# Kernel tuning notes

Measured on AMD Instinct MI355X. Metric: run time of the kernel, lower is better.

## Reference

```python
import jax, jax.numpy as jnp
import numpy as np

EDGES_1B = [[1,2],[1,39],[2,3],[2,25],[3,4],[3,18],[4,5],[4,14],[5,6],[5,8],[6,7],[6,11],[7,8],[8,9],[9,39],[10,11],[10,13],[11,12],[13,14],[14,15],[15,16],[16,17],[16,19],[16,24],[17,18],[17,27],[19,20],[19,33],[20,21],[20,34],[21,22],[22,23],[22,35],[23,24],[23,36],[25,26],[25,37],[26,27],[26,28],[26,29],[28,29],[29,38],[30,38],[31,32],[33,34],[35,36]]
NUM_GRAPHS = 8192
NODES_PER_GRAPH = 39
HIDDEN = 128
NODE_F, EDGE_F, OUT_F = 4, 2, 2
EPS = 1e-5


def _build_edge_index():
    e0 = np.array([[u - 1, v - 1] for u, v in EDGES_1B], dtype=np.int64)
    e = np.concatenate([e0, e0[:, ::-1]], axis=0).T  # [2, 92] bidirectional
    off = np.arange(NUM_GRAPHS, dtype=np.int64) * NODES_PER_GRAPH
    ei = (e[:, None, :] + off[None, :, None]).reshape(2, -1)  # [2, 8192*92]
    return jnp.asarray(ei)


def setup_inputs() -> dict:
    key = jax.random.key(0)
    ks = jax.random.split(key, 16)
    N = NUM_GRAPHS * NODES_PER_GRAPH
    E = NUM_GRAPHS * 92

    def lin(k, fi, fo):
        k1, k2 = jax.random.split(k)
        s = 1.0 / np.sqrt(fi)
        return (jax.random.uniform(k1, (fi, fo), jnp.float32, -s, s),
                jax.random.uniform(k2, (fo,), jnp.float32, -s, s))

    W1a, b1a = lin(ks[0], 2 * NODE_F + EDGE_F, HIDDEN)
    W1b, b1b = lin(ks[1], HIDDEN, HIDDEN)
    W2a, b2a = lin(ks[2], 2 * HIDDEN + EDGE_F, HIDDEN)
    W2b, b2b = lin(ks[3], HIDDEN, HIDDEN)
    Wo, bo = lin(ks[4], HIDDEN, OUT_F)
    return {
        'x': jax.random.normal(ks[5], (N, NODE_F), jnp.float32),
        'edge_index': _build_edge_index(),
        'edge_attr': jax.random.normal(ks[6], (E, EDGE_F), jnp.float32),
        'W1a': W1a, 'b1a': b1a, 'W1b': W1b, 'b1b': b1b,
        'g1': jnp.ones((HIDDEN,), jnp.float32), 'be1': jnp.zeros((HIDDEN,), jnp.float32),
        'W2a': W2a, 'b2a': b2a, 'W2b': W2b, 'b2b': b2b,
        'g2': jnp.ones((HIDDEN,), jnp.float32), 'be2': jnp.zeros((HIDDEN,), jnp.float32),
        'Wo': Wo, 'bo': bo,
    }


def _gnn_layer(x, src, dst, edge_attr, Wa, ba, Wb, bb):
    # message: mlp(cat[x_i, x_j, edge_attr]) with x_i = target, x_j = source
    m = jnp.concatenate([x[dst], x[src], edge_attr], axis=1)  # [E, 2F+Fe]
    m = jax.nn.relu(m @ Wa + ba) @ Wb + bb                    # [E, H]
    N = x.shape[0]
    agg = jax.ops.segment_sum(m, dst, num_segments=N)         # scatter-sum
    cnt = jax.ops.segment_sum(jnp.ones((m.shape[0],), m.dtype), dst, num_segments=N)
    return agg / jnp.maximum(cnt, 1.0)[:, None]               # mean aggregation


def _batch_norm(x, gamma, beta):
    mu = jnp.mean(x, axis=0)
    var = jnp.mean(jnp.square(x - mu), axis=0)  # biased var (training-mode BN)
    return (x - mu) * jax.lax.rsqrt(var + EPS) * gamma + beta


def reference(x, edge_index, edge_attr, W1a, b1a, W1b, b1b, g1, be1,
              W2a, b2a, W2b, b2b, g2, be2, Wo, bo):
    src, dst = edge_index[0], edge_index[1]
    h = _gnn_layer(x, src, dst, edge_attr, W1a, b1a, W1b, b1b)
    h = jax.nn.relu(_batch_norm(h, g1, be1))
    h = _gnn_layer(h, src, dst, edge_attr, W2a, b2a, W2b, b2b)
    h = jax.nn.relu(_batch_norm(h, g2, be2))
    return h @ Wo + bo
```

## Files before the change

### kernel.cpp

```cpp
#include <hip/hip_runtime.h>
#include <hip/hip_bf16.h>

#define NG 8192
#define NPG 39
#define H 128
#define NTOT (NG*NPG)
#define INV_N (1.0f/319488.0f)
#define SHS 136
#define ES 40

typedef __attribute__((ext_vector_type(8))) short bf16x8;
typedef __attribute__((ext_vector_type(8))) unsigned short u16x8;
typedef __attribute__((ext_vector_type(4))) float f32x4;
typedef unsigned short u16;

__device__ __forceinline__ float u16tof(u16 u) {
  union { unsigned int i; float f; } v; v.i = ((unsigned int)u) << 16; return v.f;
}
__device__ __forceinline__ u16 ftou16(float f) {
  union { float f; unsigned int i; } v; v.f = f;
  const unsigned int x = v.i;
  return (u16)((x + 0x7FFFu + ((x >> 16) & 1u)) >> 16);
}
__device__ __forceinline__ unsigned int pk2(float lo, float hi) {
  return (unsigned int)ftou16(lo) | ((unsigned int)ftou16(hi) << 16);
}

__constant__ int INC_OFF[40] = {0,2,5,8,11,14,17,19,22,24,26,29,30,32,35,37,41,44,46,49,
                                52,54,57,60,62,65,69,71,73,76,77,78,79,81,83,85,87,88,90,92};
__constant__ int INC_EID[92] = {
 46,47, 0,48,49, 2,50,51, 4,52,53, 6,54,55, 8,56,57, 10,58, 9,12,59, 13,60,
 61,62, 11,15,63, 17, 16,64, 7,18,65, 19,66, 20,67,68,69, 21,70,71, 5,24,
 22,72,73, 26,74,75, 28,76, 30,77,78, 31,79,80, 23,33, 3,81,82, 35,83,84,85,
 25,37, 38,86, 39,40,87, 88, 89, 43, 27,90, 29,44, 32,91, 34,45, 36, 41,42, 1,14};
__constant__ int INC_SRC[92] = {
 1,38, 0,2,24, 1,3,17, 2,4,13, 3,5,7, 4,6,10, 5,7, 4,6,8, 7,38,
 10,12, 5,9,11, 10, 9,13, 3,12,14, 13,15, 14,16,18,23, 15,17,26, 2,16,
 15,19,32, 18,20,33, 19,21, 20,22,34, 21,23,35, 15,22, 1,25,36, 24,26,27,28,
 16,25, 25,28, 25,27,37, 37, 31, 30, 18,33, 19,32, 21,35, 22,34, 24, 28,29, 0,8};
__constant__ int EDST[92] = {
 1,38,2,24,3,17,4,13,5,7,6,10,7,8,38,10,12,11,13,14,15,16,18,23,17,26,19,32,20,33,21,22,34,23,35,25,36,26,27,28,28,37,37,31,33,35,
 0,0,1,1,2,2,3,3,4,4,5,5,6,7,8,9,9,10,12,13,14,15,15,15,16,16,18,18,19,19,20,21,21,22,22,24,24,25,25,25,27,28,29,30,32,34};
__constant__ int ESRC[92] = {
 0,0,1,1,2,2,3,3,4,4,5,5,6,7,8,9,9,10,12,13,14,15,15,15,16,16,18,18,19,19,20,21,21,22,22,24,24,25,25,25,27,28,29,30,32,34,
 1,38,2,24,3,17,4,13,5,7,6,10,7,8,38,10,12,11,13,14,15,16,18,23,17,26,19,32,20,33,21,22,34,23,35,25,36,26,27,28,28,37,37,31,33,35};
__constant__ float DEGINV[39] = {
 0.5f, 1.f/3, 1.f/3, 1.f/3, 1.f/3, 1.f/3, 0.5f, 1.f/3, 0.5f, 0.5f,
 1.f/3, 1.f,   0.5f, 1.f/3, 0.5f, 0.25f, 1.f/3, 0.5f, 1.f/3, 1.f/3,
 0.5f, 1.f/3, 1.f/3, 0.5f, 1.f/3, 0.25f, 0.5f, 0.5f, 1.f/3, 1.f,
 1.f,  1.f,   0.5f, 0.5f, 0.5f, 0.5f, 1.f,  0.5f, 0.5f};

__global__ __launch_bounds__(256)
void k_tr(const float* __restrict__ W2a, const float* __restrict__ W2b,
          const float* __restrict__ W1b, const float* __restrict__ W1a,
          u16* __restrict__ WT)
{
  const int idx = blockIdx.x * 256 + threadIdx.x;
  if (idx < 65536) {
    const int mat = idx >> 14, rem = idx & 16383;
    const int n = rem >> 7, k = rem & 127;
    float v;
    if (mat == 0)      v = W2a[k*H + n];
    else if (mat == 1) v = W2a[(128 + k)*H + n];
    else if (mat == 2) v = W2b[k*H + n];
    else               v = W1b[k*H + n];
    WT[mat*16384 + n*128 + k] = ftou16(v);
  } else if (idx < 69632) {
    const int rem = idx - 65536;
    const int col = rem >> 5, k = rem & 31;
    const float v = (k < 10) ? W1a[k*H + col] : 0.f;
    WT[65536 + col*32 + k] = ftou16(v);
  }
}

__global__ __launch_bounds__(512, 8)
void k_layer1(const float* __restrict__ x, const float* __restrict__ ea,
              const u16* __restrict__ W1aT, const float* __restrict__ b1a,
              const u16* __restrict__ W1bT, const float* __restrict__ b1b,
              u16* __restrict__ h1, float* __restrict__ pstats)
{
  __shared__ alignas(16) u16 shb[48*SHS];
  __shared__ alignas(16) u16 msgb[92*SHS];
  __shared__ alignas(16) float sx[160];
  __shared__ alignas(16) float sea[184];
  u16* Eb = shb;
  const int g = blockIdx.x, tid = threadIdx.x;
  const int lane = tid & 63, wv = tid >> 6;
  const int qd = lane >> 4, ln = lane & 15;
  const int col = wv*16 + ln;

  for (int i = tid; i < 156; i += 512) sx[i] = x[g*156 + i];
  for (int i = tid; i < 184; i += 512) sea[i] = ea[g*184 + i];
  __syncthreads();

  if (tid < 92) {
    const int e = tid;
    const int d = EDST[e], s = ESRC[e];
    u16x8 r0, r1, z;
    r0[0] = ftou16(sx[d*4]);   r0[1] = ftou16(sx[d*4+1]);
    r0[2] = ftou16(sx[d*4+2]); r0[3] = ftou16(sx[d*4+3]);
    r0[4] = ftou16(sx[s*4]);   r0[5] = ftou16(sx[s*4+1]);
    r0[6] = ftou16(sx[s*4+2]); r0[7] = ftou16(sx[s*4+3]);
    r1[0] = ftou16(sea[e*2]);  r1[1] = ftou16(sea[e*2+1]);
    #pragma unroll
    for (int q = 2; q < 8; ++q) r1[q] = 0;
    #pragma unroll
    for (int q = 0; q < 8; ++q) z[q] = 0;
    *(u16x8*)&Eb[e*ES]      = r0;
    *(u16x8*)&Eb[e*ES + 8]  = r1;
    *(u16x8*)&Eb[e*ES + 16] = z;
    *(u16x8*)&Eb[e*ES + 24] = z;
  }
  __syncthreads();

  {
    const bf16x8 aw = *(const bf16x8*)(W1aT + col*32 + qd*8);
    const float4 bc = *(const float4*)&b1a[wv*16 + qd*4];
    #pragma unroll
    for (int et = 0; et < 6; ++et) {
      const bf16x8 be = *(const bf16x8*)&Eb[(et*16 + ln)*ES + qd*8];
      f32x4 acc = {0.f,0.f,0.f,0.f};
      acc = __builtin_amdgcn_mfma_f32_16x16x32_bf16(aw, be, acc, 0, 0, 0);
      const int e = et*16 + ln;
      if (e < 92) {
        uint2 st;
        st.x = pk2(fmaxf(acc[0] + bc.x, 0.f), fmaxf(acc[1] + bc.y, 0.f));
        st.y = pk2(fmaxf(acc[2] + bc.z, 0.f), fmaxf(acc[3] + bc.w, 0.f));
        *(uint2*)&msgb[e*SHS + wv*16 + qd*4] = st;
      }
    }
  }
  __syncthreads();

  {
    const int j2 = tid & 63;
    const int nq = tid >> 6;
    for (int n = nq; n < 39; n += 8) {
      float a0 = 0.f, a1 = 0.f;
      const int o1 = INC_OFF[n+1];
      for (int t = INC_OFF[n]; t < o1; ++t) {
        const int e = INC_EID[t];
        const ushort2 m = *(const ushort2*)&msgb[e*SHS + 2*j2];
        a0 += u16tof(m.x); a1 += u16tof(m.y);
      }
      *(unsigned int*)&shb[n*SHS + 2*j2] = pk2(a0 * DEGINV[n], a1 * DEGINV[n]);
    }
  }
  __syncthreads();

  {
    bf16x8 aw[4];
    const u16* wbp = W1bT + col*128 + qd*8;
    #pragma unroll
    for (int kt = 0; kt < 4; ++kt) aw[kt] = *(const bf16x8*)(wbp + kt*32);
    const float4 bc = *(const float4*)&b1b[wv*16 + qd*4];
    f32x4 s0 = {0.f,0.f,0.f,0.f}, s1 = {0.f,0.f,0.f,0.f};
    #pragma unroll
    for (int mt = 0; mt < 3; ++mt) {
      bf16x8 b[4];
      const u16* ap = shb + (mt*16 + ln)*SHS + qd*8;
      #pragma unroll
      for (int kt = 0; kt < 4; ++kt) b[kt] = *(const bf16x8*)(ap + kt*32);
      f32x4 acc = {0.f,0.f,0.f,0.f};
      #pragma unroll
      for (int kt = 0; kt < 4; ++kt)
        acc = __builtin_amdgcn_mfma_f32_16x16x32_bf16(aw[kt], b[kt], acc, 0, 0, 0);
      const int node = mt*16 + ln;
      if (node < 39) {
        const float v0 = acc[0] + bc.x, v1 = acc[1] + bc.y;
        const float v2 = acc[2] + bc.z, v3 = acc[3] + bc.w;
        uint2 st; st.x = pk2(v0, v1); st.y = pk2(v2, v3);
        *(uint2*)&h1[(size_t)(g*39 + node)*H + wv*16 + qd*4] = st;
        s0[0] += v0; s0[1] += v1; s0[2] += v2; s0[3] += v3;
        s1[0] += v0*v0; s1[1] += v1*v1; s1[2] += v2*v2; s1[3] += v3*v3;
      }
    }
    #pragma unroll
    for (int off = 1; off <= 8; off <<= 1) {
      #pragma unroll
      for (int r = 0; r < 4; ++r) {
        s0[r] += __shfl_xor(s0[r], off);
        s1[r] += __shfl_xor(s1[r], off);
      }
    }
    if (ln == 0) {
      *(f32x4*)&pstats[(size_t)0*NG*H + (size_t)g*H + wv*16 + qd*4] = s0;
      *(f32x4*)&pstats[(size_t)1*NG*H + (size_t)g*H + wv*16 + qd*4] = s1;
    }
  }
}

__global__ __launch_bounds__(256)
void k_red1(const float* __restrict__ pstats, float* __restrict__ part2)
{
  const int b = blockIdx.x, tid = threadIdx.x;
  const int j = tid & 127, p = tid >> 7;
  const float* base = pstats + (size_t)p*NG*H + (size_t)b*64*H + j;
  float s = 0.f;
  for (int r = 0; r < 64; ++r) s += base[r*H];
  part2[p*128*H + b*H + j] = s;
}

__global__ __launch_bounds__(256)
void k_red2(const float* __restrict__ part2, const float* __restrict__ gamma,
            const float* __restrict__ beta, float* __restrict__ sc)
{
  __shared__ float st[256];
  const int tid = threadIdx.x;
  const int j = tid & 127, p = tid >> 7;
  const float* base = part2 + p*128*H + j;
  float s = 0.f;
  for (int b = 0; b < 128; ++b) s += base[b*H];
  st[p*128 + j] = s;
  __syncthreads();
  if (tid < 128) {
    const float mu  = st[tid] * INV_N;
    const float var = st[128 + tid] * INV_N - mu*mu;
    const float inv = rsqrtf(fmaxf(var, 0.f) + 1e-5f);
    const float s1  = gamma[tid] * inv;
    sc[tid]       = s1;
    sc[128 + tid] = beta[tid] - mu * s1;
  }
}

__global__ __launch_bounds__(512, 8)
void k_layer2(const u16* __restrict__ h1, const float* __restrict__ ea,
              const float* __restrict__ sc1,
              const u16* __restrict__ WdT, const u16* __restrict__ WsT,
              const u16* __restrict__ WbT,
              const float* __restrict__ W2a, const float* __restrict__ b2a,
              const float* __restrict__ b2b,
              u16* __restrict__ h2, float* __restrict__ pstats)
{
  __shared__ alignas(16) u16 shb[48*SHS];
  __shared__ alignas(16) u16 pdb[48*SHS];
  __shared__ alignas(16) u16 psb[48*SHS];
  __shared__ alignas(16) float sea[184];
  const int g = blockIdx.x, tid = threadIdx.x;
  const int lane = tid & 63, wv = tid >> 6;
  const int qd = lane >> 4, ln = lane & 15;
  const int col = wv*16 + ln;

  for (int i = tid; i < 184; i += 512) sea[i] = ea[g*184 + i];
  {
    const u16* hp = h1 + (size_t)g*39*H;
    for (int i = tid; i < 1248; i += 512) {
      const int n = i >> 5, j = (i & 31) * 4;
      const ushort4 hv = ((const ushort4*)hp)[i];
      const float4 s0 = *(const float4*)&sc1[j];
      const float4 s1 = *(const float4*)&sc1[128 + j];
      uint2 st;
      st.x = pk2(fmaxf(u16tof(hv.x)*s0.x + s1.x, 0.f),
                 fmaxf(u16tof(hv.y)*s0.y + s1.y, 0.f));
      st.y = pk2(fmaxf(u16tof(hv.z)*s0.z + s1.z, 0.f),
                 fmaxf(u16tof(hv.w)*s0.w + s1.w, 0.f));
      *(uint2*)&shb[n*SHS + j] = st;
    }
  }
  __syncthreads();

  {
    bf16x8 ad[4], as[4];
    const u16* wdp = WdT + col*128 + qd*8;
    const u16* wsp = WsT + col*128 + qd*8;
    #pragma unroll
    for (int kt = 0; kt < 4; ++kt) {
      ad[kt] = *(const bf16x8*)(wdp + kt*32);
      as[kt] = *(const bf16x8*)(wsp + kt*32);
    }
    #pragma unroll
    for (int mt = 0; mt < 3; ++mt) {
      bf16x8 b[4];
      const u16* ap = shb + (mt*16 + ln)*SHS + qd*8;
      #pragma unroll
      for (int kt = 0; kt < 4; ++kt) b[kt] = *(const bf16x8*)(ap + kt*32);
      f32x4 accd = {0.f,0.f,0.f,0.f}, accs = {0.f,0.f,0.f,0.f};
      #pragma unroll
      for (int kt = 0; kt < 4; ++kt) {
        accd = __builtin_amdgcn_mfma_f32_16x16x32_bf16(ad[kt], b[kt], accd, 0, 0, 0);
        accs = __builtin_amdgcn_mfma_f32_16x16x32_bf16(as[kt], b[kt], accs, 0, 0, 0);
      }
      const int node = mt*16 + ln;
      if (node < 39) {
        uint2 std_, sts_;
        std_.x = pk2(accd[0], accd[1]); std_.y = pk2(accd[2], accd[3]);
        sts_.x = pk2(accs[0], accs[1]); sts_.y = pk2(accs[2], accs[3]);
        *(uint2*)&pdb[node*SHS + wv*16 + qd*4] = std_;
        *(uint2*)&psb[node*SHS + wv*16 + qd*4] = sts_;
      }
    }
  }
  __syncthreads();

  {
    const int j2 = tid & 63;
    const int nq = tid >> 6;
    const float2 w8 = *(const float2*)&W2a[256*H + 2*j2];
    const float2 w9 = *(const float2*)&W2a[257*H + 2*j2];
    const float2 b2 = *(const float2*)&b2a[2*j2];
    for (int n = nq; n < 39; n += 8) {
      const ushort2 pdu = *(const ushort2*)&pdb[n*SHS + 2*j2];
      const float base0 = u16tof(pdu.x) + b2.x;
      const float base1 = u16tof(pdu.y) + b2.y;
      float a0 = 0.f, a1 = 0.f;
      const int o1 = INC_OFF[n+1];
      for (int t = INC_OFF[n]; t < o1; ++t) {
        const int e = INC_EID[t], s = INC_SRC[t];
        const float2 se = *(const float2*)&sea[e*2];
        const ushort2 ps = *(const ushort2*)&psb[s*SHS + 2*j2];
        const float h0 = base0 + u16tof(ps.x) + se.x*w8.x + se.y*w9.x;
        const float h1v = base1 + u16tof(ps.y) + se.x*w8.y + se.y*w9.y;
        a0 += fmaxf(h0, 0.f);
        a1 += fmaxf(h1v, 0.f);
      }
      *(unsigned int*)&shb[n*SHS + 2*j2] = pk2(a0 * DEGINV[n], a1 * DEGINV[n]);
    }
  }
  __syncthreads();

  {
    bf16x8 aw[4];
    const u16* wbp = WbT + col*128 + qd*8;
    #pragma unroll
    for (int kt = 0; kt < 4; ++kt) aw[kt] = *(const bf16x8*)(wbp + kt*32);
    const float4 bc = *(const float4*)&b2b[wv*16 + qd*4];
    f32x4 s0 = {0.f,0.f,0.f,0.f}, s1 = {0.f,0.f,0.f,0.f};
    #pragma unroll
    for (int mt = 0; mt < 3; ++mt) {
      bf16x8 b[4];
      const u16* ap = shb + (mt*16 + ln)*SHS + qd*8;
      #pragma unroll
      for (int kt = 0; kt < 4; ++kt) b[kt] = *(const bf16x8*)(ap + kt*32);
      f32x4 acc = {0.f,0.f,0.f,0.f};
      #pragma unroll
      for (int kt = 0; kt < 4; ++kt)
        acc = __builtin_amdgcn_mfma_f32_16x16x32_bf16(aw[kt], b[kt], acc, 0, 0, 0);
      const int node = mt*16 + ln;
      if (node < 39) {
        const float v0 = acc[0] + bc.x, v1 = acc[1] + bc.y;
        const float v2 = acc[2] + bc.z, v3 = acc[3] + bc.w;
        uint2 st; st.x = pk2(v0, v1); st.y = pk2(v2, v3);
        *(uint2*)&h2[(size_t)(g*39 + node)*H + wv*16 + qd*4] = st;
        s0[0] += v0; s0[1] += v1; s0[2] += v2; s0[3] += v3;
        s1[0] += v0*v0; s1[1] += v1*v1; s1[2] += v2*v2; s1[3] += v3*v3;
      }
    }
    #pragma unroll
    for (int off = 1; off <= 8; off <<= 1) {
      #pragma unroll
      for (int r = 0; r < 4; ++r) {
        s0[r] += __shfl_xor(s0[r], off);
        s1[r] += __shfl_xor(s1[r], off);
      }
    }
    if (ln == 0) {
      *(f32x4*)&pstats[(size_t)0*NG*H + (size_t)g*H + wv*16 + qd*4] = s0;
      *(f32x4*)&pstats[(size_t)1*NG*H + (size_t)g*H + wv*16 + qd*4] = s1;
    }
  }
}

__global__ __launch_bounds__(256)
void k_out(const u16* __restrict__ h2, const float* __restrict__ sc2,
           const float* __restrict__ Wo, const float* __restrict__ bo,
           float* __restrict__ out)
{
  const int tid = threadIdx.x;
  const int lane = tid & 63;
  const size_t n = (size_t)blockIdx.x*4 + (tid >> 6);
  const int c = lane * 2;
  const ushort2 hv = *(const ushort2*)&h2[n*H + c];
  const float2 s0 = *(const float2*)&sc2[c];
  const float2 s1 = *(const float2*)&sc2[128 + c];
  const float v0 = fmaxf(u16tof(hv.x)*s0.x + s1.x, 0.f);
  const float v1 = fmaxf(u16tof(hv.y)*s0.y + s1.y, 0.f);
  const float4 w = *(const float4*)&Wo[c*2];
  float a0 = v0*w.x + v1*w.z;
  float a1 = v0*w.y + v1*w.w;
  #pragma unroll
  for (int off = 32; off > 0; off >>= 1) {
    a0 += __shfl_down(a0, off);
    a1 += __shfl_down(a1, off);
  }
  if (lane == 0) {
    *(float2*)&out[n*2] = make_float2(a0 + bo[0], a1 + bo[1]);
  }
}

extern "C" void kernel_launch(void* const* d_in, const int* in_sizes, int n_in,
                              void* d_out, int out_size, void* d_ws, size_t ws_size,
                              hipStream_t stream)
{
  const float* x   = (const float*)d_in[0];
  const float* ea  = (const float*)d_in[2];
  const float* W1a = (const float*)d_in[3];
  const float* b1a = (const float*)d_in[4];
  const float* W1b = (const float*)d_in[5];
  const float* b1b = (const float*)d_in[6];
  const float* g1  = (const float*)d_in[7];
  const float* be1 = (const float*)d_in[8];
  const float* W2a = (const float*)d_in[9];
  const float* b2a = (const float*)d_in[10];
  const float* W2b = (const float*)d_in[11];
  const float* b2b = (const float*)d_in[12];
  const float* g2  = (const float*)d_in[13];
  const float* be2 = (const float*)d_in[14];
  const float* Wo  = (const float*)d_in[15];
  const float* bo  = (const float*)d_in[16];
  float* out = (float*)d_out;

  char* ws = (char*)d_ws;
  size_t off = 0;
  u16* h1 = (u16*)(ws + off); off += (size_t)NTOT*H*2;
  u16* h2 = (u16*)(ws + off); off += (size_t)NTOT*H*2;
  float* pstats1 = (float*)(ws + off); off += (size_t)2*NG*H*4;
  float* pstats2 = (float*)(ws + off); off += (size_t)2*NG*H*4;
  float* p2a = (float*)(ws + off); off += (size_t)2*128*H*4;
  float* p2b = (float*)(ws + off); off += (size_t)2*128*H*4;
  float* sc1 = (float*)(ws + off); off += 256*4;
  float* sc2 = (float*)(ws + off); off += 256*4;
  u16* WT = (u16*)(ws + off); off += (size_t)(4*16384 + 4096)*2;
  u16* WdT  = WT;
  u16* WsT  = WT + 16384;
  u16* WbT  = WT + 32768;
  u16* W1bT = WT + 49152;
  u16* W1aT = WT + 65536;

  k_tr<<<272, 256, 0, stream>>>(W2a, W2b, W1b, W1a, WT);
  k_layer1<<<NG, 512, 0, stream>>>(x, ea, W1aT, b1a, W1bT, b1b, h1, pstats1);
  k_red1<<<128, 256, 0, stream>>>(pstats1, p2a);
  k_red2<<<1, 256, 0, stream>>>(p2a, g1, be1, sc1);
  k_layer2<<<NG, 512, 0, stream>>>(h1, ea, sc1, WdT, WsT, WbT, W2a, b2a, b2b, h2, pstats2);
  k_red1<<<128, 256, 0, stream>>>(pstats2, p2b);
  k_red2<<<1, 256, 0, stream>>>(p2b, g2, be2, sc2);
  k_out<<<NTOT/4, 256, 0, stream>>>(h2, sc2, Wo, bo, out);
}
```

Before: 417.9 us.

## Replace scalar edge aggregation with incidence-matrix MFMA and per-edge layer-2 messages

The per-node scatter loops in both layers are replaced by a dense 0/1 incidence matrix (built once in k_tr) multiplied on the matrix cores against transposed per-edge messages held in shared memory. Layer 2 now computes the message MLP per edge with MFMA, gathering dst and src rows through precomputed offsets, instead of precomputing per-node dst/src projections and combining them in a scalar loop. The goal is to remove irregular scalar shared-memory gathers and serial loops, at the price of redundant per-edge matmul work (96 edges vs 39 nodes) and larger shared-memory buffers. Launch bounds drop from 8 to 4 blocks per CU to fit the bigger LDS footprint, which lowers occupancy.

```diff
diff --git a/kernel.cpp b/kernel.cpp
--- a/kernel.cpp
+++ b/kernel.cpp
@@ -8,6 +8,7 @@
 #define INV_N (1.0f/319488.0f)
 #define SHS 136
 #define ES 40
+#define MTS 104
 
 typedef __attribute__((ext_vector_type(8))) short bf16x8;
 typedef __attribute__((ext_vector_type(8))) unsigned short u16x8;
@@ -26,18 +27,6 @@
   return (unsigned int)ftou16(lo) | ((unsigned int)ftou16(hi) << 16);
 }
 
-__constant__ int INC_OFF[40] = {0,2,5,8,11,14,17,19,22,24,26,29,30,32,35,37,41,44,46,49,
-                                52,54,57,60,62,65,69,71,73,76,77,78,79,81,83,85,87,88,90,92};
-__constant__ int INC_EID[92] = {
- 46,47, 0,48,49, 2,50,51, 4,52,53, 6,54,55, 8,56,57, 10,58, 9,12,59, 13,60,
- 61,62, 11,15,63, 17, 16,64, 7,18,65, 19,66, 20,67,68,69, 21,70,71, 5,24,
- 22,72,73, 26,74,75, 28,76, 30,77,78, 31,79,80, 23,33, 3,81,82, 35,83,84,85,
- 25,37, 38,86, 39,40,87, 88, 89, 43, 27,90, 29,44, 32,91, 34,45, 36, 41,42, 1,14};
-__constant__ int INC_SRC[92] = {
- 1,38, 0,2,24, 1,3,17, 2,4,13, 3,5,7, 4,6,10, 5,7, 4,6,8, 7,38,
- 10,12, 5,9,11, 10, 9,13, 3,12,14, 13,15, 14,16,18,23, 15,17,26, 2,16,
- 15,19,32, 18,20,33, 19,21, 20,22,34, 21,23,35, 15,22, 1,25,36, 24,26,27,28,
- 16,25, 25,28, 25,27,37, 37, 31, 30, 18,33, 19,32, 21,35, 22,34, 24, 28,29, 0,8};
 __constant__ int EDST[92] = {
  1,38,2,24,3,17,4,13,5,7,6,10,7,8,38,10,12,11,13,14,15,16,18,23,17,26,19,32,20,33,21,22,34,23,35,25,36,26,27,28,28,37,37,31,33,35,
  0,0,1,1,2,2,3,3,4,4,5,5,6,7,8,9,9,10,12,13,14,15,15,15,16,16,18,18,19,19,20,21,21,22,22,24,24,25,25,25,27,28,29,30,32,34};
@@ -70,17 +59,24 @@
     const int col = rem >> 5, k = rem & 31;
     const float v = (k < 10) ? W1a[k*H + col] : 0.f;
     WT[65536 + col*32 + k] = ftou16(v);
-  }
-}
-
-__global__ __launch_bounds__(512, 8)
+  } else if (idx < 74240) {
+    const int r = idx - 69632;
+    const int n = r / 96, e = r - n*96;
+    u16 v = 0;
+    if (e < 92 && EDST[e] == n) v = 0x3F80u;
+    WT[69632 + n*96 + e] = v;
+  }
+}
+
+__global__ __launch_bounds__(512, 4)
 void k_layer1(const float* __restrict__ x, const float* __restrict__ ea,
               const u16* __restrict__ W1aT, const float* __restrict__ b1a,
               const u16* __restrict__ W1bT, const float* __restrict__ b1b,
+              const u16* __restrict__ INCG,
               u16* __restrict__ h1, float* __restrict__ pstats)
 {
   __shared__ alignas(16) u16 shb[48*SHS];
-  __shared__ alignas(16) u16 msgb[92*SHS];
+  __shared__ alignas(16) u16 m1T[128*MTS];
   __shared__ alignas(16) float sx[160];
   __shared__ alignas(16) float sea[184];
   u16* Eb = shb;
@@ -110,40 +106,54 @@
     *(u16x8*)&Eb[e*ES + 8]  = r1;
     *(u16x8*)&Eb[e*ES + 16] = z;
     *(u16x8*)&Eb[e*ES + 24] = z;
-  }
-  __syncthreads();
-
-  {
-    const bf16x8 aw = *(const bf16x8*)(W1aT + col*32 + qd*8);
-    const float4 bc = *(const float4*)&b1a[wv*16 + qd*4];
+  } else if (tid < 96) {
+    u16x8 z;
+    #pragma unroll
+    for (int q = 0; q < 8; ++q) z[q] = 0;
+    *(u16x8*)&Eb[tid*ES]      = z;
+    *(u16x8*)&Eb[tid*ES + 8]  = z;
+    *(u16x8*)&Eb[tid*ES + 16] = z;
+    *(u16x8*)&Eb[tid*ES + 24] = z;
+  }
+  __syncthreads();
+
+  {
+    const bf16x8 bw1 = *(const bf16x8*)(W1aT + col*32 + qd*8);
+    const float b1c = b1a[col];
     #pragma unroll
     for (int et = 0; et < 6; ++et) {
-      const bf16x8 be = *(const bf16x8*)&Eb[(et*16 + ln)*ES + qd*8];
-      f32x4 acc = {0.f,0.f,0.f,0.f};
-      acc = __builtin_amdgcn_mfma_f32_16x16x32_bf16(aw, be, acc, 0, 0, 0);
-      const int e = et*16 + ln;
-      if (e < 92) {
+      const bf16x8 a = *(const bf16x8*)&Eb[(et*16 + ln)*ES + qd*8];
+      f32x4 acc = {0.f,0.f,0.f,0.f};
+      acc = __builtin_amdgcn_mfma_f32_16x16x32_bf16(a, bw1, acc, 0, 0, 0);
+      const int eb = et*16 + qd*4;
+      uint2 st;
+      st.x = pk2(fmaxf(acc[0] + b1c, 0.f), fmaxf(acc[1] + b1c, 0.f));
+      st.y = pk2(fmaxf(acc[2] + b1c, 0.f), fmaxf(acc[3] + b1c, 0.f));
+      *(uint2*)&m1T[col*MTS + eb] = st;
+    }
+  }
+  __syncthreads();
+
+  {
+    bf16x8 am[3];
+    #pragma unroll
+    for (int kt = 0; kt < 3; ++kt) am[kt] = *(const bf16x8*)&m1T[col*MTS + kt*32 + qd*8];
+    #pragma unroll
+    for (int mt = 0; mt < 3; ++mt) {
+      f32x4 acc = {0.f,0.f,0.f,0.f};
+      #pragma unroll
+      for (int kt = 0; kt < 3; ++kt) {
+        const bf16x8 bi = *(const bf16x8*)&INCG[(mt*16 + ln)*96 + kt*32 + qd*8];
+        acc = __builtin_amdgcn_mfma_f32_16x16x32_bf16(am[kt], bi, acc, 0, 0, 0);
+      }
+      const int node = mt*16 + ln;
+      if (node < 39) {
+        const float dg = DEGINV[node];
         uint2 st;
-        st.x = pk2(fmaxf(acc[0] + bc.x, 0.f), fmaxf(acc[1] + bc.y, 0.f));
-        st.y = pk2(fmaxf(acc[2] + bc.z, 0.f), fmaxf(acc[3] + bc.w, 0.f));
-        *(uint2*)&msgb[e*SHS + wv*16 + qd*4] = st;
-      }
-    }
-  }
-  __syncthreads();
-
-  {
-    const int j2 = tid & 63;
-    const int nq = tid >> 6;
-    for (int n = nq; n < 39; n += 8) {
-      float a0 = 0.f, a1 = 0.f;
-      const int o1 = INC_OFF[n+1];
-      for (int t = INC_OFF[n]; t < o1; ++t) {
-        const int e = INC_EID[t];
-        const ushort2 m = *(const ushort2*)&msgb[e*SHS + 2*j2];
-        a0 += u16tof(m.x); a1 += u16tof(m.y);
-      }
-      *(unsigned int*)&shb[n*SHS + 2*j2] = pk2(a0 * DEGINV[n], a1 * DEGINV[n]);
+        st.x = pk2(acc[0]*dg, acc[1]*dg);
+        st.y = pk2(acc[2]*dg, acc[3]*dg);
+        *(uint2*)&shb[node*SHS + wv*16 + qd*4] = st;
+      }
     }
   }
   __syncthreads();
@@ -223,25 +233,30 @@
   }
 }
 
-__global__ __launch_bounds__(512, 8)
+__global__ __launch_bounds__(512, 4)
 void k_layer2(const u16* __restrict__ h1, const float* __restrict__ ea,
               const float* __restrict__ sc1,
               const u16* __restrict__ WdT, const u16* __restrict__ WsT,
               const u16* __restrict__ WbT,
               const float* __restrict__ W2a, const float* __restrict__ b2a,
-              const float* __restrict__ b2b,
+              const float* __restrict__ b2b, const u16* __restrict__ INCG,
               u16* __restrict__ h2, float* __restrict__ pstats)
 {
   __shared__ alignas(16) u16 shb[48*SHS];
-  __shared__ alignas(16) u16 pdb[48*SHS];
-  __shared__ alignas(16) u16 psb[48*SHS];
+  __shared__ alignas(16) u16 m2T[128*MTS];
   __shared__ alignas(16) float sea[184];
+  __shared__ int sdo[96], sso[96];
   const int g = blockIdx.x, tid = threadIdx.x;
   const int lane = tid & 63, wv = tid >> 6;
   const int qd = lane >> 4, ln = lane & 15;
   const int col = wv*16 + ln;
 
   for (int i = tid; i < 184; i += 512) sea[i] = ea[g*184 + i];
+  if (tid < 96) {
+    const int e = (tid < 92) ? tid : 91;
+    sdo[tid] = EDST[e]*SHS;
+    sso[tid] = ESRC[e]*SHS;
+  }
   {
     const u16* hp = h1 + (size_t)g*39*H;
     for (int i = tid; i < 1248; i += 512) {
@@ -260,60 +275,66 @@
   __syncthreads();
 
   {
-    bf16x8 ad[4], as[4];
+    bf16x8 bwd[4], bws[4];
     const u16* wdp = WdT + col*128 + qd*8;
     const u16* wsp = WsT + col*128 + qd*8;
     #pragma unroll
     for (int kt = 0; kt < 4; ++kt) {
-      ad[kt] = *(const bf16x8*)(wdp + kt*32);
-      as[kt] = *(const bf16x8*)(wsp + kt*32);
-    }
+      bwd[kt] = *(const bf16x8*)(wdp + kt*32);
+      bws[kt] = *(const bf16x8*)(wsp + kt*32);
+    }
+    const float w8c = W2a[256*H + col];
+    const float w9c = W2a[257*H + col];
+    const float b2c = b2a[col];
+    #pragma unroll
+    for (int et = 0; et < 6; ++et) {
+      const int dofs = sdo[et*16 + ln];
+      const int sofs = sso[et*16 + ln];
+      f32x4 acc = {0.f,0.f,0.f,0.f};
+      #pragma unroll
+      for (int kt = 0; kt < 4; ++kt) {
+        const bf16x8 a = *(const bf16x8*)&shb[dofs + kt*32 + qd*8];
+        acc = __builtin_amdgcn_mfma_f32_16x16x32_bf16(a, bwd[kt], acc, 0, 0, 0);
+      }
+      #pragma unroll
+      for (int kt = 0; kt < 4; ++kt) {
+        const bf16x8 a = *(const bf16x8*)&shb[sofs + kt*32 + qd*8];
+        acc = __builtin_amdgcn_mfma_f32_16x16x32_bf16(a, bws[kt], acc, 0, 0, 0);
+      }
+      const int eb = et*16 + qd*4;
+      float v[4];
+      #pragma unroll
+      for (int r = 0; r < 4; ++r) {
+        const int er = (eb + r < 92) ? (eb + r) : 91;
+        const float2 se = *(const float2*)&sea[er*2];
+        v[r] = fmaxf(acc[r] + b2c + se.x*w8c + se.y*w9c, 0.f);
+      }
+      uint2 st; st.x = pk2(v[0], v[1]); st.y = pk2(v[2], v[3]);
+      *(uint2*)&m2T[col*MTS + eb] = st;
+    }
+  }
+  __syncthreads();
+
+  {
+    bf16x8 am[3];
+    #pragma unroll
+    for (int kt = 0; kt < 3; ++kt) am[kt] = *(const bf16x8*)&m2T[col*MTS + kt*32 + qd*8];
     #pragma unroll
     for (int mt = 0; mt < 3; ++mt) {
-      bf16x8 b[4];
-      const u16* ap = shb + (mt*16 + ln)*SHS + qd*8;
-      #pragma unroll
-      for (int kt = 0; kt < 4; ++kt) b[kt] = *(const bf16x8*)(ap + kt*32);
-      f32x4 accd = {0.f,0.f,0.f,0.f}, accs = {0.f,0.f,0.f,0.f};
-      #pragma unroll
-      for (int kt = 0; kt < 4; ++kt) {
-        accd = __builtin_amdgcn_mfma_f32_16x16x32_bf16(ad[kt], b[kt], accd, 0, 0, 0);
-        accs = __builtin_amdgcn_mfma_f32_16x16x32_bf16(as[kt], b[kt], accs, 0, 0, 0);
+      f32x4 acc = {0.f,0.f,0.f,0.f};
+      #pragma unroll
+      for (int kt = 0; kt < 3; ++kt) {
+        const bf16x8 bi = *(const bf16x8*)&INCG[(mt*16 + ln)*96 + kt*32 + qd*8];
+        acc = __builtin_amdgcn_mfma_f32_16x16x32_bf16(am[kt], bi, acc, 0, 0, 0);
       }
       const int node = mt*16 + ln;
       if (node < 39) {
-        uint2 std_, sts_;
-        std_.x = pk2(accd[0], accd[1]); std_.y = pk2(accd[2], accd[3]);
-        sts_.x = pk2(accs[0], accs[1]); sts_.y = pk2(accs[2], accs[3]);
-        *(uint2*)&pdb[node*SHS + wv*16 + qd*4] = std_;
-        *(uint2*)&psb[node*SHS + wv*16 + qd*4] = sts_;
-      }
-    }
-  }
-  __syncthreads();
-
-  {
-    const int j2 = tid & 63;
-    const int nq = tid >> 6;
-    const float2 w8 = *(const float2*)&W2a[256*H + 2*j2];
-    const float2 w9 = *(const float2*)&W2a[257*H + 2*j2];
-    const float2 b2 = *(const float2*)&b2a[2*j2];
-    for (int n = nq; n < 39; n += 8) {
-      const ushort2 pdu = *(const ushort2*)&pdb[n*SHS + 2*j2];
-      const float base0 = u16tof(pdu.x) + b2.x;
-      const float base1 = u16tof(pdu.y) + b2.y;
-      float a0 = 0.f, a1 = 0.f;
-      const int o1 = INC_OFF[n+1];
-      for (int t = INC_OFF[n]; t < o1; ++t) {
-        const int e = INC_EID[t], s = INC_SRC[t];
-        const float2 se = *(const float2*)&sea[e*2];
-        const ushort2 ps = *(const ushort2*)&psb[s*SHS + 2*j2];
-        const float h0 = base0 + u16tof(ps.x) + se.x*w8.x + se.y*w9.x;
-        const float h1v = base1 + u16tof(ps.y) + se.x*w8.y + se.y*w9.y;
-        a0 += fmaxf(h0, 0.f);
-        a1 += fmaxf(h1v, 0.f);
-      }
-      *(unsigned int*)&shb[n*SHS + 2*j2] = pk2(a0 * DEGINV[n], a1 * DEGINV[n]);
+        const float dg = DEGINV[node];
+        uint2 st;
+        st.x = pk2(acc[0]*dg, acc[1]*dg);
+        st.y = pk2(acc[2]*dg, acc[3]*dg);
+        *(uint2*)&shb[node*SHS + wv*16 + qd*4] = st;
+      }
     }
   }
   __syncthreads();
@@ -419,18 +440,19 @@
   float* p2b = (float*)(ws + off); off += (size_t)2*128*H*4;
   float* sc1 = (float*)(ws + off); off += 256*4;
   float* sc2 = (float*)(ws + off); off += 256*4;
-  u16* WT = (u16*)(ws + off); off += (size_t)(4*16384 + 4096)*2;
+  u16* WT = (u16*)(ws + off); off += (size_t)(4*16384 + 4096 + 4608)*2;
   u16* WdT  = WT;
   u16* WsT  = WT + 16384;
   u16* WbT  = WT + 32768;
   u16* W1bT = WT + 49152;
   u16* W1aT = WT + 65536;
-
-  k_tr<<<272, 256, 0, stream>>>(W2a, W2b, W1b, W1a, WT);
-  k_layer1<<<NG, 512, 0, stream>>>(x, ea, W1aT, b1a, W1bT, b1b, h1, pstats1);
+  u16* INCG = WT + 69632;
+
+  k_tr<<<290, 256, 0, stream>>>(W2a, W2b, W1b, W1a, WT);
+  k_layer1<<<NG, 512, 0, stream>>>(x, ea, W1aT, b1a, W1bT, b1b, INCG, h1, pstats1);
   k_red1<<<128, 256, 0, stream>>>(pstats1, p2a);
   k_red2<<<1, 256, 0, stream>>>(p2a, g1, be1, sc1);
-  k_layer2<<<NG, 512, 0, stream>>>(h1, ea, sc1, WdT, WsT, WbT, W2a, b2a, b2b, h2, pstats2);
+  k_layer2<<<NG, 512, 0, stream>>>(h1, ea, sc1, WdT, WsT, WbT, W2a, b2a, b2b, INCG, h2, pstats2);
   k_red1<<<128, 256, 0, stream>>>(pstats2, p2b);
   k_red2<<<1, 256, 0, stream>>>(p2b, g2, be2, sc2);
   k_out<<<NTOT/4, 256, 0, stream>>>(h2, sc2, Wo, bo, out);
```

New measurement: 434.1 us. 3.9% more time.
